# Optimization experiments

Measured on AMD Instinct MI355X. Metric: run time of the kernel, lower is better.

The kernel has to match this reference:

```python
import jax, jax.numpy as jnp
import numpy as np

B, T, K, N, D = 4, 1024, 3, 4, 64
TIME_SCALES = [1, 2, 4]  # sorted, scale 1 included; N = lcm = 4
PHASE = 1


def _build_routing_tables(phase):
    # PhaseTables._build_stream_head_maps, SHARED assignment, single phase
    stream_ids = np.arange(N)
    s2h = np.empty((K, N), dtype=np.int32)
    h2s = np.empty((K, N), dtype=np.int32)
    for k, s in enumerate(TIME_SCALES):
        alpha = N // s
        j = phase % s
        row = (stream_ids + alpha * j) % N
        s2h[k] = row
        inv = np.empty_like(row)
        inv[row] = stream_ids
        h2s[k] = inv
    return jnp.asarray(s2h), jnp.asarray(h2s)


def setup_inputs() -> dict:
    key = jax.random.key(0)
    kx, kw = jax.random.split(key)
    x = jax.random.normal(kx, (B, T, K, N, D), dtype=jnp.float32)
    # trunc_normal_init_ with std = 1/sqrt(in_dim); plain normal*std is a faithful stand-in
    Wqkv = jax.random.normal(kw, (K, N, D, 3 * D), dtype=jnp.float32) * (1.0 / D ** 0.5)
    s2h, h2s = _build_routing_tables(PHASE)
    return {"x": x, "Wqkv": Wqkv, "stream_to_head": s2h, "head_to_stream": h2s}


def _route_n(x_btkni, idx_kn):
    # out[b,t,k,n,i] = x[b,t,k,idx_kn[k,n],i]  (torch.gather along dim=3)
    k_idx = jnp.arange(K)[:, None]  # [K,1] broadcasts with idx_kn [K,N]
    return x_btkni[:, :, k_idx, idx_kn, :]


def _forward(x, Wqkv, stream_to_head, head_to_stream):
    # SLOT-scope SHARED projection: streams -> heads, grouped projection, heads -> streams
    x_head = _route_n(x, head_to_stream)                       # [B,T,K,N,D]
    qkv_head = jnp.einsum('btkni,knio->btkno', x_head, Wqkv)   # [B,T,K,N,3D]
    qkv = _route_n(qkv_head, stream_to_head)                   # stream order

    # AttentionAdapter (SDPA, causal, dropout_p=0, no rope)
    H = K * N
    qkv = qkv.reshape(B, T, H, 3, D)
    q = qkv[..., 0, :].transpose(0, 2, 1, 3)  # [B,H,T,D]
    k = qkv[..., 1, :].transpose(0, 2, 1, 3)
    v = qkv[..., 2, :].transpose(0, 2, 1, 3)
    scale = 1.0 / jnp.sqrt(jnp.asarray(D, dtype=q.dtype))
    scores = jnp.einsum('bhtd,bhsd->bhts', q, k) * scale       # [B,H,T,T]
    causal = jnp.tril(jnp.ones((T, T), dtype=bool))
    scores = jnp.where(causal, scores, jnp.finfo(scores.dtype).min)
    probs = jax.nn.softmax(scores, axis=-1)
    out_bhtd = jnp.einsum('bhts,bhsd->bhtd', probs, v)          # [B,H,T,D]
    # reshape to [B,K,N,T,D] then permute -> [B,T,K,N,D]
    out = out_bhtd.reshape(B, K, N, T, D).transpose(0, 3, 1, 2, 4)
    return out


def reference(x, Wqkv, stream_to_head, head_to_stream):
    return _forward(x, Wqkv, stream_to_head, head_to_stream)
```

## Files before the change

### kernel.cpp

```cpp
#include <hip/hip_runtime.h>

using f32x4 = __attribute__((ext_vector_type(4))) float;
using s16x8 = __attribute__((ext_vector_type(8))) short;

constexpr int B = 4, T = 1024, Kk = 3, Nn = 4, H = 12, D = 64;
constexpr int LDK = 72;

__device__ __forceinline__ short f2bf(float f) {
    unsigned u = __float_as_uint(f);
    u = (u + 0x7fffu + ((u >> 16) & 1u)) >> 16;
    return (short)u;
}

__global__ __launch_bounds__(256) void proj_kernel(
    const float* __restrict__ x, const float* __restrict__ W,
    const int* __restrict__ s2h,
    short* __restrict__ qw, short* __restrict__ kw, short* __restrict__ vt)
{
    __shared__ short ax[64 * LDK];
    __shared__ short wt[192 * LDK];
    const int h = blockIdx.y;
    const int kk = h / Nn;
    const int m = s2h[h];
    const float* Wp = W + (size_t)(kk * Nn + m) * D * 192;
    const int tid = threadIdx.x;
    const int t0g = blockIdx.x * 64;
    const int b = t0g / T, t0 = t0g % T;
    const int bh = b * H + h;

    const float* xp = x + ((size_t)(b * T + t0) * H + h) * D;
    for (int e4 = tid; e4 < 64 * 16; e4 += 256) {
        int row = e4 >> 4, i4 = e4 & 15;
        float4 v = *reinterpret_cast<const float4*>(xp + (size_t)row * H * D + i4 * 4);
        *reinterpret_cast<short4*>(&ax[row * LDK + i4 * 4]) =
            make_short4(f2bf(v.x), f2bf(v.y), f2bf(v.z), f2bf(v.w));
    }
    for (int e4 = tid; e4 < 64 * 48; e4 += 256) {
        int i = e4 / 48, o0 = (e4 % 48) * 4;
        float4 v = *reinterpret_cast<const float4*>(Wp + (size_t)i * 192 + o0);
        wt[(o0 + 0) * LDK + i] = f2bf(v.x);
        wt[(o0 + 1) * LDK + i] = f2bf(v.y);
        wt[(o0 + 2) * LDK + i] = f2bf(v.z);
        wt[(o0 + 3) * LDK + i] = f2bf(v.w);
    }
    __syncthreads();

    const int wv = tid >> 6, lane = tid & 63, quad = lane >> 4, c = lane & 15;
    s16x8 af[4][2];
    #pragma unroll
    for (int mb = 0; mb < 4; ++mb)
        #pragma unroll
        for (int ks = 0; ks < 2; ++ks)
            af[mb][ks] = *reinterpret_cast<const s16x8*>(
                &ax[(mb * 16 + c) * LDK + ks * 32 + quad * 8]);

    f32x4 acc[4][3];
    #pragma unroll
    for (int mb = 0; mb < 4; ++mb)
        #pragma unroll
        for (int nb = 0; nb < 3; ++nb)
            acc[mb][nb] = (f32x4){0.f, 0.f, 0.f, 0.f};

    #pragma unroll
    for (int nb = 0; nb < 3; ++nb) {
        const int o16 = wv * 3 + nb;
        #pragma unroll
        for (int ks = 0; ks < 2; ++ks) {
            s16x8 bf = *reinterpret_cast<const s16x8*>(
                &wt[(o16 * 16 + c) * LDK + ks * 32 + quad * 8]);
            #pragma unroll
            for (int mb = 0; mb < 4; ++mb)
                acc[mb][nb] = __builtin_amdgcn_mfma_f32_16x16x32_bf16(
                    af[mb][ks], bf, acc[mb][nb], 0, 0, 0);
        }
    }

    #pragma unroll
    for (int nb = 0; nb < 3; ++nb) {
        const int o = (wv * 3 + nb) * 16 + c;
        const int part = o >> 6, d = o & 63;
        #pragma unroll
        for (int mb = 0; mb < 4; ++mb) {
            #pragma unroll
            for (int reg = 0; reg < 4; ++reg) {
                const int t = t0 + mb * 16 + quad * 4 + reg;
                const short val = f2bf(acc[mb][nb][reg]);
                if (part == 0)      qw[((size_t)bh * T + t) * D + d] = val;
                else if (part == 1) kw[((size_t)bh * T + t) * D + d] = val;
                else                vt[((size_t)bh * D + d) * T + t] = val;
            }
        }
    }
}

__global__ __launch_bounds__(256) void attn_kernel(
    const short* __restrict__ qw, const short* __restrict__ kw,
    const short* __restrict__ vt, float* __restrict__ out)
{
    __shared__ short lk[64 * LDK];
    __shared__ short lv[64 * LDK];
    __shared__ short lp[4][16 * LDK];

    const int idx = blockIdx.x;
    const int bh = idx % (B * H);
    const int qi = idx / (B * H);
    const int qt = (qi & 1) ? (qi >> 1) : (15 - (qi >> 1));
    const int b = bh / H, h = bh % H;
    const int tid = threadIdx.x, wv = tid >> 6, lane = tid & 63;
    const int quad = lane >> 4, c = lane & 15;
    const int tq0 = qt * 64;

    s16x8 qf[2];
    {
        const short* qp = qw + ((size_t)bh * T + tq0 + wv * 16 + c) * D;
        qf[0] = *reinterpret_cast<const s16x8*>(qp + quad * 8);
        qf[1] = *reinterpret_cast<const s16x8*>(qp + 32 + quad * 8);
    }

    f32x4 oacc[4];
    #pragma unroll
    for (int cb = 0; cb < 4; ++cb) oacc[cb] = (f32x4){0.f, 0.f, 0.f, 0.f};
    float m_run[4], l_run[4];
    #pragma unroll
    for (int r = 0; r < 4; ++r) { m_run[r] = -1e30f; l_run[r] = 0.f; }

    for (int st = 0; st <= qt; ++st) {
        __syncthreads();
        const short* kp = kw + ((size_t)bh * T + st * 64) * D;
        const short* vp = vt + (size_t)bh * D * T + st * 64;
        for (int e8 = tid; e8 < 512; e8 += 256) {
            const int row = e8 >> 3, c8 = e8 & 7;
            *reinterpret_cast<uint4*>(&lk[row * LDK + c8 * 8]) =
                *reinterpret_cast<const uint4*>(kp + (size_t)row * D + c8 * 8);
            *reinterpret_cast<uint4*>(&lv[row * LDK + c8 * 8]) =
                *reinterpret_cast<const uint4*>(vp + (size_t)row * T + c8 * 8);
        }
        __syncthreads();

        f32x4 sacc[4];
        #pragma unroll
        for (int cb = 0; cb < 4; ++cb) sacc[cb] = (f32x4){0.f, 0.f, 0.f, 0.f};
        #pragma unroll
        for (int ks = 0; ks < 2; ++ks) {
            #pragma unroll
            for (int cb = 0; cb < 4; ++cb) {
                s16x8 bf = *reinterpret_cast<const s16x8*>(
                    &lk[(cb * 16 + c) * LDK + ks * 32 + quad * 8]);
                sacc[cb] = __builtin_amdgcn_mfma_f32_16x16x32_bf16(
                    qf[ks], bf, sacc[cb], 0, 0, 0);
            }
        }

        float ps[4][4];
        #pragma unroll
        for (int cb = 0; cb < 4; ++cb)
            #pragma unroll
            for (int reg = 0; reg < 4; ++reg) {
                float s = sacc[cb][reg] * 0.125f;
                if (st == qt) {
                    const int col = st * 64 + cb * 16 + c;
                    const int row = tq0 + wv * 16 + quad * 4 + reg;
                    if (col > row) s = -1e30f;
                }
                ps[cb][reg] = s;
            }

        float mx[4];
        #pragma unroll
        for (int reg = 0; reg < 4; ++reg)
            mx[reg] = fmaxf(fmaxf(ps[0][reg], ps[1][reg]), fmaxf(ps[2][reg], ps[3][reg]));
        #pragma unroll
        for (int off = 1; off <= 8; off <<= 1)
            #pragma unroll
            for (int reg = 0; reg < 4; ++reg)
                mx[reg] = fmaxf(mx[reg], __shfl_xor(mx[reg], off));

        float alpha[4], lsum[4];
        #pragma unroll
        for (int reg = 0; reg < 4; ++reg) {
            const float m_new = fmaxf(m_run[reg], mx[reg]);
            alpha[reg] = __expf(m_run[reg] - m_new);
            m_run[reg] = m_new;
            lsum[reg] = 0.f;
        }
        #pragma unroll
        for (int cb = 0; cb < 4; ++cb)
            #pragma unroll
            for (int reg = 0; reg < 4; ++reg) {
                const float p = __expf(ps[cb][reg] - m_run[reg]);
                ps[cb][reg] = p;
                lsum[reg] += p;
                lp[wv][(quad * 4 + reg) * LDK + cb * 16 + c] = f2bf(p);
            }
        #pragma unroll
        for (int off = 1; off <= 8; off <<= 1)
            #pragma unroll
            for (int reg = 0; reg < 4; ++reg)
                lsum[reg] += __shfl_xor(lsum[reg], off);
        #pragma unroll
        for (int reg = 0; reg < 4; ++reg)
            l_run[reg] = alpha[reg] * l_run[reg] + lsum[reg];
        #pragma unroll
        for (int cb = 0; cb < 4; ++cb)
            #pragma unroll
            for (int reg = 0; reg < 4; ++reg)
                oacc[cb][reg] *= alpha[reg];

        #pragma unroll
        for (int ks = 0; ks < 2; ++ks) {
            s16x8 af = *reinterpret_cast<const s16x8*>(
                &lp[wv][c * LDK + ks * 32 + quad * 8]);
            #pragma unroll
            for (int cb = 0; cb < 4; ++cb) {
                s16x8 bf = *reinterpret_cast<const s16x8*>(
                    &lv[(cb * 16 + c) * LDK + ks * 32 + quad * 8]);
                oacc[cb] = __builtin_amdgcn_mfma_f32_16x16x32_bf16(
                    af, bf, oacc[cb], 0, 0, 0);
            }
        }
    }

    float inv_l[4];
    #pragma unroll
    for (int reg = 0; reg < 4; ++reg) inv_l[reg] = 1.0f / l_run[reg];
    #pragma unroll
    for (int cb = 0; cb < 4; ++cb)
        #pragma unroll
        for (int reg = 0; reg < 4; ++reg) {
            const int t = tq0 + wv * 16 + quad * 4 + reg;
            const int d = cb * 16 + c;
            out[((size_t)(b * T + t) * H + h) * D + d] = oacc[cb][reg] * inv_l[reg];
        }
}

extern "C" void kernel_launch(void* const* d_in, const int* in_sizes, int n_in,
                              void* d_out, int out_size, void* d_ws, size_t ws_size,
                              hipStream_t stream) {
    const float* x   = (const float*)d_in[0];
    const float* W   = (const float*)d_in[1];
    const int*   s2h = (const int*)d_in[2];
    float* out = (float*)d_out;

    short* qw = (short*)d_ws;
    short* kw = qw + (size_t)B * H * T * D;
    short* vt = kw + (size_t)B * H * T * D;

    proj_kernel<<<dim3(B * T / 64, H), 256, 0, stream>>>(x, W, s2h, qw, kw, vt);
    attn_kernel<<<dim3((T / 64) * (B * H)), 256, 0, stream>>>(qw, kw, vt, out);
}
```

Before: 122.4 us.

## Pre-transform weights once, fold softmax scale into Q, widen KV tiles to 128

Adds a small kernel that transposes and converts the routed weights to bf16 once, folding the 1/sqrt(D)*log2(e) scale into the Q columns. The projection then loads these with coalesced vector copies and writes Q and V transposed with short4 stores. Attention processes 128-key chunks per iteration, uses exp2 and truncating bf16 conversion for probabilities, and gathers Q from the transposed layout. The aim is fewer loop iterations and barriers and cheaper softmax, at the cost of an extra launch, more LDS, more wasted masked work on the diagonal chunk, and slightly reduced precision.

```diff
diff --git a/kernel.cpp b/kernel.cpp
--- a/kernel.cpp
+++ b/kernel.cpp
@@ -3,26 +3,44 @@
 using f32x4 = __attribute__((ext_vector_type(4))) float;
 using s16x8 = __attribute__((ext_vector_type(8))) short;
 
-constexpr int B = 4, T = 1024, Kk = 3, Nn = 4, H = 12, D = 64;
+constexpr int B = 4, T = 1024, H = 12, D = 64;
 constexpr int LDK = 72;
+constexpr int LDV = 136;
 
 __device__ __forceinline__ short f2bf(float f) {
     unsigned u = __float_as_uint(f);
     u = (u + 0x7fffu + ((u >> 16) & 1u)) >> 16;
     return (short)u;
 }
+__device__ __forceinline__ short f2bf_trunc(float f) {
+    return (short)(__float_as_uint(f) >> 16);
+}
+
+__global__ __launch_bounds__(256) void wprep_kernel(
+    const float* __restrict__ W, const int* __restrict__ s2h,
+    short* __restrict__ wt_ws)
+{
+    const int h = blockIdx.x;
+    const int kk = h >> 2;
+    const int m = s2h[h];
+    const float* Wp = W + (size_t)(kk * 4 + m) * D * 192;
+    short* op = wt_ws + (size_t)h * 192 * D;
+    const float qs = 0.125f * 1.44269504f;
+    for (int e = threadIdx.x; e < 192 * D; e += 256) {
+        const int o = e >> 6, i = e & 63;
+        float v = Wp[(size_t)i * 192 + o];
+        if (o < 64) v *= qs;
+        op[o * 64 + i] = f2bf(v);
+    }
+}
 
 __global__ __launch_bounds__(256) void proj_kernel(
-    const float* __restrict__ x, const float* __restrict__ W,
-    const int* __restrict__ s2h,
-    short* __restrict__ qw, short* __restrict__ kw, short* __restrict__ vt)
+    const float* __restrict__ x, const short* __restrict__ wt_ws,
+    short* __restrict__ qt, short* __restrict__ kw, short* __restrict__ vt)
 {
     __shared__ short ax[64 * LDK];
     __shared__ short wt[192 * LDK];
     const int h = blockIdx.y;
-    const int kk = h / Nn;
-    const int m = s2h[h];
-    const float* Wp = W + (size_t)(kk * Nn + m) * D * 192;
     const int tid = threadIdx.x;
     const int t0g = blockIdx.x * 64;
     const int b = t0g / T, t0 = t0g % T;
@@ -30,18 +48,16 @@
 
     const float* xp = x + ((size_t)(b * T + t0) * H + h) * D;
     for (int e4 = tid; e4 < 64 * 16; e4 += 256) {
-        int row = e4 >> 4, i4 = e4 & 15;
+        const int row = e4 >> 4, i4 = e4 & 15;
         float4 v = *reinterpret_cast<const float4*>(xp + (size_t)row * H * D + i4 * 4);
         *reinterpret_cast<short4*>(&ax[row * LDK + i4 * 4]) =
             make_short4(f2bf(v.x), f2bf(v.y), f2bf(v.z), f2bf(v.w));
     }
-    for (int e4 = tid; e4 < 64 * 48; e4 += 256) {
-        int i = e4 / 48, o0 = (e4 % 48) * 4;
-        float4 v = *reinterpret_cast<const float4*>(Wp + (size_t)i * 192 + o0);
-        wt[(o0 + 0) * LDK + i] = f2bf(v.x);
-        wt[(o0 + 1) * LDK + i] = f2bf(v.y);
-        wt[(o0 + 2) * LDK + i] = f2bf(v.z);
-        wt[(o0 + 3) * LDK + i] = f2bf(v.w);
+    const short* wtp = wt_ws + (size_t)h * 192 * D;
+    for (int e8 = tid; e8 < 192 * 8; e8 += 256) {
+        const int row = e8 >> 3, c8 = e8 & 7;
+        *reinterpret_cast<uint4*>(&wt[row * LDK + c8 * 8]) =
+            *reinterpret_cast<const uint4*>(wtp + (size_t)row * 64 + c8 * 8);
     }
     __syncthreads();
 
@@ -63,7 +79,7 @@
 
     #pragma unroll
     for (int nb = 0; nb < 3; ++nb) {
-        const int o16 = wv * 3 + nb;
+        const int o16 = nb * 4 + wv;
         #pragma unroll
         for (int ks = 0; ks < 2; ++ks) {
             s16x8 bf = *reinterpret_cast<const s16x8*>(
@@ -75,47 +91,53 @@
         }
     }
 
-    #pragma unroll
-    for (int nb = 0; nb < 3; ++nb) {
-        const int o = (wv * 3 + nb) * 16 + c;
-        const int part = o >> 6, d = o & 63;
-        #pragma unroll
-        for (int mb = 0; mb < 4; ++mb) {
-            #pragma unroll
-            for (int reg = 0; reg < 4; ++reg) {
-                const int t = t0 + mb * 16 + quad * 4 + reg;
-                const short val = f2bf(acc[mb][nb][reg]);
-                if (part == 0)      qw[((size_t)bh * T + t) * D + d] = val;
-                else if (part == 1) kw[((size_t)bh * T + t) * D + d] = val;
-                else                vt[((size_t)bh * D + d) * T + t] = val;
-            }
+    const int d = wv * 16 + c;
+    #pragma unroll
+    for (int mb = 0; mb < 4; ++mb) {
+        const int t = t0 + mb * 16 + quad * 4;
+        {
+            short4 s = make_short4(f2bf(acc[mb][0][0]), f2bf(acc[mb][0][1]),
+                                   f2bf(acc[mb][0][2]), f2bf(acc[mb][0][3]));
+            *reinterpret_cast<short4*>(qt + ((size_t)bh * 64 + d) * T + t) = s;
+        }
+        #pragma unroll
+        for (int reg = 0; reg < 4; ++reg)
+            kw[((size_t)bh * T + t + reg) * D + d] = f2bf(acc[mb][1][reg]);
+        {
+            short4 s = make_short4(f2bf(acc[mb][2][0]), f2bf(acc[mb][2][1]),
+                                   f2bf(acc[mb][2][2]), f2bf(acc[mb][2][3]));
+            *reinterpret_cast<short4*>(vt + ((size_t)bh * 64 + d) * T + t) = s;
         }
     }
 }
 
 __global__ __launch_bounds__(256) void attn_kernel(
-    const short* __restrict__ qw, const short* __restrict__ kw,
+    const short* __restrict__ qt_ws, const short* __restrict__ kw,
     const short* __restrict__ vt, float* __restrict__ out)
 {
-    __shared__ short lk[64 * LDK];
-    __shared__ short lv[64 * LDK];
-    __shared__ short lp[4][16 * LDK];
+    __shared__ short lk[128 * LDK];
+    __shared__ short lv[64 * LDV];
+    __shared__ short lp[4][16 * LDV];
 
     const int idx = blockIdx.x;
     const int bh = idx % (B * H);
     const int qi = idx / (B * H);
-    const int qt = (qi & 1) ? (qi >> 1) : (15 - (qi >> 1));
+    const int qtile = (qi & 1) ? (qi >> 1) : (15 - (qi >> 1));
     const int b = bh / H, h = bh % H;
     const int tid = threadIdx.x, wv = tid >> 6, lane = tid & 63;
     const int quad = lane >> 4, c = lane & 15;
-    const int tq0 = qt * 64;
-
+    const int tq0 = qtile * 64;
+
+    short qfr[2][8];
+    #pragma unroll
+    for (int ks = 0; ks < 2; ++ks)
+        #pragma unroll
+        for (int j = 0; j < 8; ++j)
+            qfr[ks][j] = qt_ws[((size_t)bh * 64 + ks * 32 + quad * 8 + j) * T
+                               + tq0 + wv * 16 + c];
     s16x8 qf[2];
-    {
-        const short* qp = qw + ((size_t)bh * T + tq0 + wv * 16 + c) * D;
-        qf[0] = *reinterpret_cast<const s16x8*>(qp + quad * 8);
-        qf[1] = *reinterpret_cast<const s16x8*>(qp + 32 + quad * 8);
-    }
+    qf[0] = *reinterpret_cast<const s16x8*>(qfr[0]);
+    qf[1] = *reinterpret_cast<const s16x8*>(qfr[1]);
 
     f32x4 oacc[4];
     #pragma unroll
@@ -124,51 +146,56 @@
     #pragma unroll
     for (int r = 0; r < 4; ++r) { m_run[r] = -1e30f; l_run[r] = 0.f; }
 
-    for (int st = 0; st <= qt; ++st) {
+    const int nch = (qtile + 2) >> 1;
+    for (int ch = 0; ch < nch; ++ch) {
         __syncthreads();
-        const short* kp = kw + ((size_t)bh * T + st * 64) * D;
-        const short* vp = vt + (size_t)bh * D * T + st * 64;
-        for (int e8 = tid; e8 < 512; e8 += 256) {
-            const int row = e8 >> 3, c8 = e8 & 7;
-            *reinterpret_cast<uint4*>(&lk[row * LDK + c8 * 8]) =
-                *reinterpret_cast<const uint4*>(kp + (size_t)row * D + c8 * 8);
-            *reinterpret_cast<uint4*>(&lv[row * LDK + c8 * 8]) =
-                *reinterpret_cast<const uint4*>(vp + (size_t)row * T + c8 * 8);
+        const short* kp = kw + ((size_t)bh * T + ch * 128) * D;
+        const short* vp = vt + (size_t)bh * 64 * T + ch * 128;
+        for (int e8 = tid; e8 < 1024; e8 += 256) {
+            const int r = e8 >> 3, c8 = e8 & 7;
+            *reinterpret_cast<uint4*>(&lk[r * LDK + c8 * 8]) =
+                *reinterpret_cast<const uint4*>(kp + (size_t)r * D + c8 * 8);
+        }
+        for (int e8 = tid; e8 < 1024; e8 += 256) {
+            const int r = e8 >> 4, c8 = e8 & 15;
+            *reinterpret_cast<uint4*>(&lv[r * LDV + c8 * 8]) =
+                *reinterpret_cast<const uint4*>(vp + (size_t)r * T + c8 * 8);
         }
         __syncthreads();
 
-        f32x4 sacc[4];
-        #pragma unroll
-        for (int cb = 0; cb < 4; ++cb) sacc[cb] = (f32x4){0.f, 0.f, 0.f, 0.f};
-        #pragma unroll
-        for (int ks = 0; ks < 2; ++ks) {
-            #pragma unroll
-            for (int cb = 0; cb < 4; ++cb) {
+        f32x4 sacc[8];
+        #pragma unroll
+        for (int cb = 0; cb < 8; ++cb) sacc[cb] = (f32x4){0.f, 0.f, 0.f, 0.f};
+        #pragma unroll
+        for (int ks = 0; ks < 2; ++ks)
+            #pragma unroll
+            for (int cb = 0; cb < 8; ++cb) {
                 s16x8 bf = *reinterpret_cast<const s16x8*>(
                     &lk[(cb * 16 + c) * LDK + ks * 32 + quad * 8]);
                 sacc[cb] = __builtin_amdgcn_mfma_f32_16x16x32_bf16(
                     qf[ks], bf, sacc[cb], 0, 0, 0);
             }
-        }
-
-        float ps[4][4];
-        #pragma unroll
-        for (int cb = 0; cb < 4; ++cb)
-            #pragma unroll
-            for (int reg = 0; reg < 4; ++reg) {
-                float s = sacc[cb][reg] * 0.125f;
-                if (st == qt) {
-                    const int col = st * 64 + cb * 16 + c;
+
+        if (ch == nch - 1) {
+            #pragma unroll
+            for (int cb = 0; cb < 8; ++cb)
+                #pragma unroll
+                for (int reg = 0; reg < 4; ++reg) {
+                    const int col = ch * 128 + cb * 16 + c;
                     const int row = tq0 + wv * 16 + quad * 4 + reg;
-                    if (col > row) s = -1e30f;
+                    if (col > row) sacc[cb][reg] = -1e30f;
                 }
-                ps[cb][reg] = s;
-            }
+        }
 
         float mx[4];
         #pragma unroll
-        for (int reg = 0; reg < 4; ++reg)
-            mx[reg] = fmaxf(fmaxf(ps[0][reg], ps[1][reg]), fmaxf(ps[2][reg], ps[3][reg]));
+        for (int reg = 0; reg < 4; ++reg) {
+            float m0 = fmaxf(fmaxf(sacc[0][reg], sacc[1][reg]),
+                             fmaxf(sacc[2][reg], sacc[3][reg]));
+            float m1 = fmaxf(fmaxf(sacc[4][reg], sacc[5][reg]),
+                             fmaxf(sacc[6][reg], sacc[7][reg]));
+            mx[reg] = fmaxf(m0, m1);
+        }
         #pragma unroll
         for (int off = 1; off <= 8; off <<= 1)
             #pragma unroll
@@ -179,18 +206,17 @@
         #pragma unroll
         for (int reg = 0; reg < 4; ++reg) {
             const float m_new = fmaxf(m_run[reg], mx[reg]);
-            alpha[reg] = __expf(m_run[reg] - m_new);
+            alpha[reg] = __builtin_amdgcn_exp2f(m_run[reg] - m_new);
             m_run[reg] = m_new;
             lsum[reg] = 0.f;
         }
         #pragma unroll
-        for (int cb = 0; cb < 4; ++cb)
+        for (int cb = 0; cb < 8; ++cb)
             #pragma unroll
             for (int reg = 0; reg < 4; ++reg) {
-                const float p = __expf(ps[cb][reg] - m_run[reg]);
-                ps[cb][reg] = p;
+                const float p = __builtin_amdgcn_exp2f(sacc[cb][reg] - m_run[reg]);
                 lsum[reg] += p;
-                lp[wv][(quad * 4 + reg) * LDK + cb * 16 + c] = f2bf(p);
+                lp[wv][(quad * 4 + reg) * LDV + cb * 16 + c] = f2bf_trunc(p);
             }
         #pragma unroll
         for (int off = 1; off <= 8; off <<= 1)
@@ -207,13 +233,13 @@
                 oacc[cb][reg] *= alpha[reg];
 
         #pragma unroll
-        for (int ks = 0; ks < 2; ++ks) {
+        for (int ks2 = 0; ks2 < 4; ++ks2) {
             s16x8 af = *reinterpret_cast<const s16x8*>(
-                &lp[wv][c * LDK + ks * 32 + quad * 8]);
+                &lp[wv][c * LDV + ks2 * 32 + quad * 8]);
             #pragma unroll
             for (int cb = 0; cb < 4; ++cb) {
                 s16x8 bf = *reinterpret_cast<const s16x8*>(
-                    &lv[(cb * 16 + c) * LDK + ks * 32 + quad * 8]);
+                    &lv[(cb * 16 + c) * LDV + ks2 * 32 + quad * 8]);
                 oacc[cb] = __builtin_amdgcn_mfma_f32_16x16x32_bf16(
                     af, bf, oacc[cb], 0, 0, 0);
             }
@@ -241,10 +267,12 @@
     const int*   s2h = (const int*)d_in[2];
     float* out = (float*)d_out;
 
-    short* qw = (short*)d_ws;
-    short* kw = qw + (size_t)B * H * T * D;
-    short* vt = kw + (size_t)B * H * T * D;
-
-    proj_kernel<<<dim3(B * T / 64, H), 256, 0, stream>>>(x, W, s2h, qw, kw, vt);
-    attn_kernel<<<dim3((T / 64) * (B * H)), 256, 0, stream>>>(qw, kw, vt, out);
-}
+    short* wt_ws = (short*)d_ws;
+    short* qt_ws = wt_ws + (size_t)12 * 192 * 64;
+    short* kw    = qt_ws + (size_t)B * H * 64 * T;
+    short* vt    = kw    + (size_t)B * H * T * 64;
+
+    wprep_kernel<<<dim3(H), 256, 0, stream>>>(W, s2h, wt_ws);
+    proj_kernel<<<dim3(B * T / 64, H), 256, 0, stream>>>(x, wt_ws, qt_ws, kw, vt);
+    attn_kernel<<<dim3((T / 64) * (B * H)), 256, 0, stream>>>(qt_ws, kw, vt, out);
+}
```

After: 119.7 us. -2.2%, faster.
